# Kernel optimization log

Measured on AMD Instinct MI355X. Metric: run time of the kernel, lower is better.

## Reference

```python
import jax, jax.numpy as jnp
import numpy as np
from jax.experimental.ode import odeint

RTOL, ATOL = 1e-4, 1e-5


def setup_inputs() -> dict:
    key = jax.random.key(0)
    ks = jax.random.split(key, 8)
    B, T = 16384, 256

    def lin(k, fan_in, fan_out):
        return jax.random.normal(k, (fan_in, fan_out), jnp.float32) / np.sqrt(fan_in)

    return {
        "x": jax.random.normal(ks[0], (B, T, 9), jnp.float32),
        "We1": lin(ks[1], 9, 64), "be1": jnp.zeros((64,), jnp.float32),
        "We2": lin(ks[2], 64, 64), "be2": jnp.zeros((64,), jnp.float32),
        "We3": lin(ks[3], 64, 2), "be3": jnp.zeros((2,), jnp.float32),
        "Wo1": lin(ks[4], 2, 32), "bo1": jnp.zeros((32,), jnp.float32),
        "Wo2": lin(ks[5], 32, 2), "bo2": jnp.zeros((2,), jnp.float32),
        "Wd": lin(ks[6], 2, 3), "bd": jnp.zeros((3,), jnp.float32),
    }


def reference(x, We1, be1, We2, be2, We3, be3, Wo1, bo1, Wo2, bo2, Wd, bd):
    B, T, C = x.shape
    # Encoder: 9 -> 64 -> 64 -> 2 (ReLU) on the first time-step only
    h = jax.nn.relu(x[:, 0, :] @ We1 + be1)
    h = jax.nn.relu(h @ We2 + be2)
    z0 = h @ We3 + be3                      # (B, 2)

    t_span = jnp.linspace(0.0, 1.0, T)      # default t_span in forward()

    # Autonomous tanh-MLP vector field: 2 -> 32 -> 2
    def vf(z, t, Wo1, bo1, Wo2, bo2):
        return jnp.tanh(z @ Wo1 + bo1) @ Wo2 + bo2

    # Adaptive dopri5, matching torchdiffeq's odeint(method='dopri5')
    z_traj = odeint(vf, z0, t_span, Wo1, bo1, Wo2, bo2, rtol=RTOL, atol=ATOL)  # (T, B, 2)

    x_hat = z_traj @ Wd + bd                # (T, B, 3) linear decoder
    return (z0, z_traj, x_hat)
```

## Files before the change

kernel.cpp:

```cpp
#include <hip/hip_runtime.h>


constexpr int   BATCH = 16384;
constexpr int   NSEG  = 12;
constexpr float DT    = 1.0f / (float)NSEG;
constexpr float DT2   = DT * 0.5f;
constexpr float DT6   = DT / 6.0f;
constexpr float SCALE = 2.8853900817779268f;
constexpr float K255  = (float)NSEG / 255.0f;

__device__ __forceinline__ float fast_exp2(float x) {
#if __has_builtin(__builtin_amdgcn_exp2f)
  return __builtin_amdgcn_exp2f(x);
#else
  return exp2f(x);
#endif
}

__device__ __forceinline__ float fast_rcp(float x) {
#if __has_builtin(__builtin_amdgcn_rcpf)
  return __builtin_amdgcn_rcpf(x);
#else
  return 1.0f / x;
#endif
}

template<int CTRL>
__device__ __forceinline__ float dpp_add(float v) {
  int sw = __builtin_amdgcn_update_dpp(0, __float_as_int(v), CTRL, 0xF, 0xF, true);
  return v + __int_as_float(sw);
}

__device__ __forceinline__ float allred16(float v) {
  v = dpp_add<0xB1>(v);
  v = dpp_add<0x4E>(v);
  v = dpp_add<0x141>(v);
  v = dpp_add<0x140>(v);
  return v;
}

__global__ __launch_bounds__(256) void gait_all(
    const float* __restrict__ x,
    const float* __restrict__ We1, const float* __restrict__ be1,
    const float* __restrict__ We2, const float* __restrict__ be2,
    const float* __restrict__ We3, const float* __restrict__ be3,
    const float* __restrict__ Wo1, const float* __restrict__ bo1,
    const float* __restrict__ Wo2, const float* __restrict__ bo2,
    const float* __restrict__ Wd,  const float* __restrict__ bd,
    float* __restrict__ out)
{
  const int tid = threadIdx.x;
  const int t   = blockIdx.x * 256 + tid;
  const int b   = t >> 4;
  const int sub = t & 15;
  const int sg  = tid >> 4;

  __shared__ float4 bndl[NSEG + 1][16];

  const float* xb = x + (size_t)b * 2304;
  float xv[9];
#pragma unroll
  for (int i = 0; i < 9; ++i) xv[i] = xb[i];

  const int c0 = sub * 4;
  float s0 = be2[c0+0], s1 = be2[c0+1], s2 = be2[c0+2], s3 = be2[c0+3];
#pragma unroll 4
  for (int i = 0; i < 64; ++i) {
    float h = be1[i];
#pragma unroll
    for (int j = 0; j < 9; ++j) h = fmaf(xv[j], We1[j*64 + i], h);
    h = fmaxf(h, 0.0f);
    const float* w2r = We2 + i*64 + c0;
    s0 = fmaf(h, w2r[0], s0);
    s1 = fmaf(h, w2r[1], s1);
    s2 = fmaf(h, w2r[2], s2);
    s3 = fmaf(h, w2r[3], s3);
  }
  s0 = fmaxf(s0, 0.0f); s1 = fmaxf(s1, 0.0f);
  s2 = fmaxf(s2, 0.0f); s3 = fmaxf(s3, 0.0f);
  float z0a = fmaf(s0, We3[(c0+0)*2+0], fmaf(s1, We3[(c0+1)*2+0],
              fmaf(s2, We3[(c0+2)*2+0],      s3 * We3[(c0+3)*2+0])));
  float z0b = fmaf(s0, We3[(c0+0)*2+1], fmaf(s1, We3[(c0+1)*2+1],
              fmaf(s2, We3[(c0+2)*2+1],      s3 * We3[(c0+3)*2+1])));
  z0a = allred16(z0a) + be3[0];
  z0b = allred16(z0b) + be3[1];

  if (sub == 5) {
    float2 v; v.x = z0a; v.y = z0b;
    *reinterpret_cast<float2*>(out + (size_t)b * 2) = v;
  }

  float w1a[2], w1b[2], b1s[2], w2a[2], w2b[2];
  const int u0 = sub * 2;
#pragma unroll
  for (int q = 0; q < 2; ++q) {
    w1a[q] = Wo1[      u0 + q] * SCALE;
    w1b[q] = Wo1[32 +  u0 + q] * SCALE;
    b1s[q] = bo1[      u0 + q] * SCALE;
    w2a[q] = Wo2[(u0 + q)*2 + 0];
    w2b[q] = Wo2[(u0 + q)*2 + 1];
  }
  const float a0i = (sub == 0) ? bo2[0] : 0.0f;
  const float a1i = (sub == 0) ? bo2[1] : 0.0f;

  auto vf = [&](float za, float zb, float& o0, float& o1) {
    float a0 = a0i, a1 = a1i;
#pragma unroll
    for (int q = 0; q < 2; ++q) {
      float u  = fmaf(za, w1a[q], fmaf(zb, w1b[q], b1s[q]));
      float e  = fast_exp2(u);
      float rr = fast_rcp(e + 1.0f);
      float th = fmaf(-2.0f, rr, 1.0f);
      a0 = fmaf(th, w2a[q], a0);
      a1 = fmaf(th, w2b[q], a1);
    }
    o0 = allred16(a0);
    o1 = allred16(a1);
  };

  float za = z0a, zb = z0b;
  float fa, fb;
  vf(za, zb, fa, fb);

  const bool storer = (sub == 0);

#pragma unroll 1
  for (int k = 0; k < NSEG; ++k) {
    if (storer) { float4 v; v.x = za; v.y = zb; v.z = fa; v.w = fb;
                  bndl[k][sg] = v; }
    float k2a, k2b, k3a, k3b, k4a, k4b, fna, fnb;
    vf(fmaf(DT2, fa,  za), fmaf(DT2, fb,  zb), k2a, k2b);
    vf(fmaf(DT2, k2a, za), fmaf(DT2, k2b, zb), k3a, k3b);
    vf(fmaf(DT,  k3a, za), fmaf(DT,  k3b, zb), k4a, k4b);
    float zna = fmaf(DT6, fa + k4a + 2.0f*(k2a + k3a), za);
    float znb = fmaf(DT6, fb + k4b + 2.0f*(k2b + k3b), zb);
    vf(zna, znb, fna, fnb);
    za = zna; zb = znb; fa = fna; fb = fnb;
  }
  if (storer) { float4 v; v.x = za; v.y = zb; v.z = fa; v.w = fb;
                bndl[NSEG][sg] = v; }

  __syncthreads();

  const float wd0 = Wd[0], wd1 = Wd[1], wd2 = Wd[2];
  const float wd3 = Wd[3], wd4 = Wd[4], wd5 = Wd[5];
  const float bd0 = bd[0], bd1 = bd[1], bd2 = bd[2];

  const int s     = tid & 15;
  const int mpart = tid >> 4;
  const int gb    = blockIdx.x * 16 + s;

  float* __restrict__ zt = out + 32768;
  float* __restrict__ xh = out + 32768 + 8388608;

#pragma unroll 1
  for (int it = 0; it < 16; ++it) {
    const int m = mpart + (it << 4);
    int k = (m * NSEG) / 255;
    if (k > NSEG - 1) k = NSEG - 1;
    const float th = fmaf((float)m, K255, -(float)k);

    const float4 p0 = bndl[k][s];
    const float4 p1 = bndl[k + 1][s];

    const float fadt  = DT * p0.z, fbdt  = DT * p0.w;
    const float fnadt = DT * p1.z, fnbdt = DT * p1.w;
    const float da = p1.x - p0.x, db = p1.y - p0.y;
    const float c2a = fmaf(3.f, da, -fmaf(2.f, fadt, fnadt));
    const float c3a = fmaf(-2.f, da, fadt + fnadt);
    const float c2b = fmaf(3.f, db, -fmaf(2.f, fbdt, fnbdt));
    const float c3b = fmaf(-2.f, db, fbdt + fnbdt);

    const float va = fmaf(fmaf(fmaf(c3a, th, c2a), th, fadt), th, p0.x);
    const float vb = fmaf(fmaf(fmaf(c3b, th, c2b), th, fbdt), th, p0.y);

    float2 zv; zv.x = va; zv.y = vb;
    *reinterpret_cast<float2*>(zt + ((size_t)m << 15) + 2 * gb) = zv;

    float* q = xh + (size_t)m * 49152 + 3 * gb;
    q[0] = fmaf(va, wd0, fmaf(vb, wd3, bd0));
    q[1] = fmaf(va, wd1, fmaf(vb, wd4, bd1));
    q[2] = fmaf(va, wd2, fmaf(vb, wd5, bd2));
  }
}

extern "C" void kernel_launch(void* const* d_in, const int* in_sizes, int n_in,
                              void* d_out, int out_size, void* d_ws, size_t ws_size,
                              hipStream_t stream)
{
  const float* x   = (const float*)d_in[0];
  const float* We1 = (const float*)d_in[1];
  const float* be1 = (const float*)d_in[2];
  const float* We2 = (const float*)d_in[3];
  const float* be2 = (const float*)d_in[4];
  const float* We3 = (const float*)d_in[5];
  const float* be3 = (const float*)d_in[6];
  const float* Wo1 = (const float*)d_in[7];
  const float* bo1 = (const float*)d_in[8];
  const float* Wo2 = (const float*)d_in[9];
  const float* bo2 = (const float*)d_in[10];
  const float* Wd  = (const float*)d_in[11];
  const float* bd  = (const float*)d_in[12];

  dim3 grid(BATCH * 16 / 256), block(256);
  gait_all<<<grid, block, 0, stream>>>(x, We1, be1, We2, be2, We3, be3,
                                       Wo1, bo1, Wo2, bo2, Wd, bd,
                                       (float*)d_out);
}
```

Measured before the change: 32.84 us.

## Process two batch samples per 16-lane group to interleave ODE dependency chains

Each 16-lane group now encodes and integrates two batch elements, with the vector field evaluated for both at once so the exp/rcp/DPP reduction chains interleave and hide latency. The grid is halved, and the output phase covers 32 samples per block with a 32x8 thread mapping. This trades fewer waves and lower occupancy, plus more registers, for more instruction-level parallelism. Output store coalescing also changes, with wider contiguous runs per timestep.

```diff
diff --git a/kernel.cpp b/kernel.cpp
--- a/kernel.cpp
+++ b/kernel.cpp
@@ -50,44 +50,48 @@
     float* __restrict__ out)
 {
   const int tid = threadIdx.x;
-  const int t   = blockIdx.x * 256 + tid;
-  const int b   = t >> 4;
-  const int sub = t & 15;
-  const int sg  = tid >> 4;
-
-  __shared__ float4 bndl[NSEG + 1][16];
-
-  const float* xb = x + (size_t)b * 2304;
-  float xv[9];
-#pragma unroll
-  for (int i = 0; i < 9; ++i) xv[i] = xb[i];
+  const int g   = tid >> 4;
+  const int sub = tid & 15;
+  const int b0  = blockIdx.x * 32 + g * 2;
+
+  __shared__ float4 bndl[NSEG + 1][32];
 
   const int c0 = sub * 4;
-  float s0 = be2[c0+0], s1 = be2[c0+1], s2 = be2[c0+2], s3 = be2[c0+3];
+  auto encode = [&](int b, float& z0a, float& z0b) {
+    const float* xb = x + (size_t)b * 2304;
+    float xv[9];
+#pragma unroll
+    for (int i = 0; i < 9; ++i) xv[i] = xb[i];
+    float s0 = be2[c0+0], s1 = be2[c0+1], s2 = be2[c0+2], s3 = be2[c0+3];
 #pragma unroll 4
-  for (int i = 0; i < 64; ++i) {
-    float h = be1[i];
-#pragma unroll
-    for (int j = 0; j < 9; ++j) h = fmaf(xv[j], We1[j*64 + i], h);
-    h = fmaxf(h, 0.0f);
-    const float* w2r = We2 + i*64 + c0;
-    s0 = fmaf(h, w2r[0], s0);
-    s1 = fmaf(h, w2r[1], s1);
-    s2 = fmaf(h, w2r[2], s2);
-    s3 = fmaf(h, w2r[3], s3);
-  }
-  s0 = fmaxf(s0, 0.0f); s1 = fmaxf(s1, 0.0f);
-  s2 = fmaxf(s2, 0.0f); s3 = fmaxf(s3, 0.0f);
-  float z0a = fmaf(s0, We3[(c0+0)*2+0], fmaf(s1, We3[(c0+1)*2+0],
-              fmaf(s2, We3[(c0+2)*2+0],      s3 * We3[(c0+3)*2+0])));
-  float z0b = fmaf(s0, We3[(c0+0)*2+1], fmaf(s1, We3[(c0+1)*2+1],
-              fmaf(s2, We3[(c0+2)*2+1],      s3 * We3[(c0+3)*2+1])));
-  z0a = allred16(z0a) + be3[0];
-  z0b = allred16(z0b) + be3[1];
+    for (int i = 0; i < 64; ++i) {
+      float h = be1[i];
+#pragma unroll
+      for (int j = 0; j < 9; ++j) h = fmaf(xv[j], We1[j*64 + i], h);
+      h = fmaxf(h, 0.0f);
+      const float* w2r = We2 + i*64 + c0;
+      s0 = fmaf(h, w2r[0], s0);
+      s1 = fmaf(h, w2r[1], s1);
+      s2 = fmaf(h, w2r[2], s2);
+      s3 = fmaf(h, w2r[3], s3);
+    }
+    s0 = fmaxf(s0, 0.0f); s1 = fmaxf(s1, 0.0f);
+    s2 = fmaxf(s2, 0.0f); s3 = fmaxf(s3, 0.0f);
+    z0a = fmaf(s0, We3[(c0+0)*2+0], fmaf(s1, We3[(c0+1)*2+0],
+          fmaf(s2, We3[(c0+2)*2+0],      s3 * We3[(c0+3)*2+0])));
+    z0b = fmaf(s0, We3[(c0+0)*2+1], fmaf(s1, We3[(c0+1)*2+1],
+          fmaf(s2, We3[(c0+2)*2+1],      s3 * We3[(c0+3)*2+1])));
+    z0a = allred16(z0a) + be3[0];
+    z0b = allred16(z0b) + be3[1];
+  };
+
+  float zA, wA, zB, wB;
+  encode(b0,     zA, wA);
+  encode(b0 + 1, zB, wB);
 
   if (sub == 5) {
-    float2 v; v.x = z0a; v.y = z0b;
-    *reinterpret_cast<float2*>(out + (size_t)b * 2) = v;
+    float4 v; v.x = zA; v.y = wA; v.z = zB; v.w = wB;
+    *reinterpret_cast<float4*>(out + (size_t)b0 * 2) = v;
   }
 
   float w1a[2], w1b[2], b1s[2], w2a[2], w2b[2];
@@ -103,42 +107,58 @@
   const float a0i = (sub == 0) ? bo2[0] : 0.0f;
   const float a1i = (sub == 0) ? bo2[1] : 0.0f;
 
-  auto vf = [&](float za, float zb, float& o0, float& o1) {
-    float a0 = a0i, a1 = a1i;
+  auto vf2 = [&](float zaA, float zbA, float zaB, float zbB,
+                 float& oA0, float& oA1, float& oB0, float& oB1) {
+    float A0 = a0i, A1 = a1i, B0 = a0i, B1 = a1i;
 #pragma unroll
     for (int q = 0; q < 2; ++q) {
-      float u  = fmaf(za, w1a[q], fmaf(zb, w1b[q], b1s[q]));
-      float e  = fast_exp2(u);
-      float rr = fast_rcp(e + 1.0f);
-      float th = fmaf(-2.0f, rr, 1.0f);
-      a0 = fmaf(th, w2a[q], a0);
-      a1 = fmaf(th, w2b[q], a1);
+      float uA  = fmaf(zaA, w1a[q], fmaf(zbA, w1b[q], b1s[q]));
+      float uB  = fmaf(zaB, w1a[q], fmaf(zbB, w1b[q], b1s[q]));
+      float eA  = fast_exp2(uA);
+      float eB  = fast_exp2(uB);
+      float rA  = fast_rcp(eA + 1.0f);
+      float rB  = fast_rcp(eB + 1.0f);
+      float tA  = fmaf(-2.0f, rA, 1.0f);
+      float tB  = fmaf(-2.0f, rB, 1.0f);
+      A0 = fmaf(tA, w2a[q], A0);  B0 = fmaf(tB, w2a[q], B0);
+      A1 = fmaf(tA, w2b[q], A1);  B1 = fmaf(tB, w2b[q], B1);
     }
-    o0 = allred16(a0);
-    o1 = allred16(a1);
+    oA0 = allred16(A0);  oB0 = allred16(B0);
+    oA1 = allred16(A1);  oB1 = allred16(B1);
   };
 
-  float za = z0a, zb = z0b;
-  float fa, fb;
-  vf(za, zb, fa, fb);
+  float fA0, fA1, fB0, fB1;
+  vf2(zA, wA, zB, wB, fA0, fA1, fB0, fB1);
 
   const bool storer = (sub == 0);
+  const int  sA = g * 2, sB = sA + 1;
 
 #pragma unroll 1
   for (int k = 0; k < NSEG; ++k) {
-    if (storer) { float4 v; v.x = za; v.y = zb; v.z = fa; v.w = fb;
-                  bndl[k][sg] = v; }
-    float k2a, k2b, k3a, k3b, k4a, k4b, fna, fnb;
-    vf(fmaf(DT2, fa,  za), fmaf(DT2, fb,  zb), k2a, k2b);
-    vf(fmaf(DT2, k2a, za), fmaf(DT2, k2b, zb), k3a, k3b);
-    vf(fmaf(DT,  k3a, za), fmaf(DT,  k3b, zb), k4a, k4b);
-    float zna = fmaf(DT6, fa + k4a + 2.0f*(k2a + k3a), za);
-    float znb = fmaf(DT6, fb + k4b + 2.0f*(k2b + k3b), zb);
-    vf(zna, znb, fna, fnb);
-    za = zna; zb = znb; fa = fna; fb = fnb;
-  }
-  if (storer) { float4 v; v.x = za; v.y = zb; v.z = fa; v.w = fb;
-                bndl[NSEG][sg] = v; }
+    if (storer) {
+      float4 v; v.x = zA; v.y = wA; v.z = fA0; v.w = fA1; bndl[k][sA] = v;
+      float4 u; u.x = zB; u.y = wB; u.z = fB0; u.w = fB1; bndl[k][sB] = u;
+    }
+    float k2A0,k2A1,k2B0,k2B1, k3A0,k3A1,k3B0,k3B1, k4A0,k4A1,k4B0,k4B1;
+    float fnA0,fnA1,fnB0,fnB1;
+    vf2(fmaf(DT2,fA0,zA), fmaf(DT2,fA1,wA), fmaf(DT2,fB0,zB), fmaf(DT2,fB1,wB),
+        k2A0,k2A1,k2B0,k2B1);
+    vf2(fmaf(DT2,k2A0,zA), fmaf(DT2,k2A1,wA), fmaf(DT2,k2B0,zB), fmaf(DT2,k2B1,wB),
+        k3A0,k3A1,k3B0,k3B1);
+    vf2(fmaf(DT,k3A0,zA), fmaf(DT,k3A1,wA), fmaf(DT,k3B0,zB), fmaf(DT,k3B1,wB),
+        k4A0,k4A1,k4B0,k4B1);
+    float znA0 = fmaf(DT6, fA0 + k4A0 + 2.0f*(k2A0 + k3A0), zA);
+    float znA1 = fmaf(DT6, fA1 + k4A1 + 2.0f*(k2A1 + k3A1), wA);
+    float znB0 = fmaf(DT6, fB0 + k4B0 + 2.0f*(k2B0 + k3B0), zB);
+    float znB1 = fmaf(DT6, fB1 + k4B1 + 2.0f*(k2B1 + k3B1), wB);
+    vf2(znA0, znA1, znB0, znB1, fnA0, fnA1, fnB0, fnB1);
+    zA = znA0; wA = znA1; fA0 = fnA0; fA1 = fnA1;
+    zB = znB0; wB = znB1; fB0 = fnB0; fB1 = fnB1;
+  }
+  if (storer) {
+    float4 v; v.x = zA; v.y = wA; v.z = fA0; v.w = fA1; bndl[NSEG][sA] = v;
+    float4 u; u.x = zB; u.y = wB; u.z = fB0; u.w = fB1; bndl[NSEG][sB] = u;
+  }
 
   __syncthreads();
 
@@ -146,16 +166,16 @@
   const float wd3 = Wd[3], wd4 = Wd[4], wd5 = Wd[5];
   const float bd0 = bd[0], bd1 = bd[1], bd2 = bd[2];
 
-  const int s     = tid & 15;
-  const int mpart = tid >> 4;
-  const int gb    = blockIdx.x * 16 + s;
+  const int s     = tid & 31;
+  const int mpart = tid >> 5;
+  const int gb    = blockIdx.x * 32 + s;
 
   float* __restrict__ zt = out + 32768;
   float* __restrict__ xh = out + 32768 + 8388608;
 
 #pragma unroll 1
-  for (int it = 0; it < 16; ++it) {
-    const int m = mpart + (it << 4);
+  for (int it = 0; it < 32; ++it) {
+    const int m = mpart + (it << 3);
     int k = (m * NSEG) / 255;
     if (k > NSEG - 1) k = NSEG - 1;
     const float th = fmaf((float)m, K255, -(float)k);
@@ -202,7 +222,7 @@
   const float* Wd  = (const float*)d_in[11];
   const float* bd  = (const float*)d_in[12];
 
-  dim3 grid(BATCH * 16 / 256), block(256);
+  dim3 grid(BATCH / 32), block(256);
   gait_all<<<grid, block, 0, stream>>>(x, We1, be1, We2, be2, We3, be3,
                                        Wo1, bo1, Wo2, bo2, Wd, bd,
                                        (float*)d_out);
```

Result: slower. 38.65 us (+17.7%).
